# Performance work log

Measured on AMD Instinct MI355X. Metric: run time of the kernel, lower is better.

Reference implementation:

```python
import jax, jax.numpy as jnp
import numpy as np

HEADS = 4
DIM_HEAD = 32
HIDDEN = HEADS * DIM_HEAD  # 128
DIM = 128
RANK = 4
SCALING = 1.0 / RANK       # alpha / rank
SCALE = DIM_HEAD ** -0.5


def conv1x1(x, w, b=None):
    # x: [b,c,H,W], w: [o,c] (1x1 conv kernel squeezed)
    y = jnp.einsum('bcxy,oc->boxy', x, w)
    if b is not None:
        y = y + b[None, :, None, None]
    return y


def setup_inputs() -> dict:
    key = jax.random.key(0)
    ks = jax.random.split(key, 16)
    x = jax.random.normal(ks[0], (16, DIM, 64, 64), dtype=jnp.float32)
    w_qkv = jax.random.normal(ks[1], (3 * HIDDEN, DIM), dtype=jnp.float32) * 0.05
    def lora(kA, kB, kb):
        wA = jax.random.normal(kA, (RANK, DIM), dtype=jnp.float32) / RANK
        bA = jax.random.normal(kB, (RANK,), dtype=jnp.float32) * 0.01
        wB = jax.random.normal(kb, (HIDDEN, RANK), dtype=jnp.float32) * 0.05
        bB = jnp.zeros((HIDDEN,), dtype=jnp.float32)
        return wA, bA, wB, bB
    wA_q, bA_q, wB_q, bB_q = lora(ks[2], ks[3], ks[4])
    wA_k, bA_k, wB_k, bB_k = lora(ks[5], ks[6], ks[7])
    wA_v, bA_v, wB_v, bB_v = lora(ks[8], ks[9], ks[10])
    w_out = jax.random.normal(ks[11], (DIM, HIDDEN), dtype=jnp.float32) * 0.05
    b_out = jnp.zeros((DIM,), dtype=jnp.float32)
    return dict(x=x, w_qkv=w_qkv,
                wA_q=wA_q, bA_q=bA_q, wB_q=wB_q, bB_q=bB_q,
                wA_k=wA_k, bA_k=bA_k, wB_k=wB_k, bB_k=bB_k,
                wA_v=wA_v, bA_v=bA_v, wB_v=wB_v, bB_v=bB_v,
                w_out=w_out, b_out=b_out)


def reference(x, w_qkv, wA_q, bA_q, wB_q, bB_q, wA_k, bA_k, wB_k, bB_k,
              wA_v, bA_v, wB_v, bB_v, w_out, b_out):
    b, c, H, W = x.shape
    n = H * W
    qkv = conv1x1(x, w_qkv)  # [b, 3*HIDDEN, H, W]
    q0, k0, v0 = jnp.split(qkv, 3, axis=1)
    def lora_fwd(wA, bA, wB, bB):
        return conv1x1(conv1x1(x, wA, bA), wB, bB)
    q = q0 + lora_fwd(wA_q, bA_q, wB_q, bB_q) * SCALING
    k = k0 + lora_fwd(wA_k, bA_k, wB_k, bB_k) * SCALING
    v = v0 + lora_fwd(wA_v, bA_v, wB_v, bB_v) * SCALING
    # b (h c) x y -> b h c n
    def split_heads(t):
        return t.reshape(b, HEADS, DIM_HEAD, n)
    q, k, v = split_heads(q), split_heads(k), split_heads(v)
    q = jax.nn.softmax(q, axis=-2) * SCALE   # softmax over channel dim
    k = jax.nn.softmax(k, axis=-1)           # softmax over spatial dim
    v = v / n
    context = jnp.einsum('bhdn,bhen->bhde', k, v)
    out = jnp.einsum('bhde,bhdn->bhen', context, q)  # [b,h,e,n]
    out = out.reshape(b, HIDDEN, H, W)
    return conv1x1(out, w_out, b_out)
```

## Files before the change

### kernel.cpp

```cpp
#include <hip/hip_runtime.h>


typedef float f32x4 __attribute__((ext_vector_type(4)));
typedef short bf16x8 __attribute__((ext_vector_type(8)));

#define SCALING 0.25f
#define SCALE   0.17677669529663687f
#define NCHUNK  64

__device__ __forceinline__ unsigned short f2bf_rn(float x) {
    union { float f; unsigned u; } v; v.f = x;
    unsigned r = v.u + 0x7FFFu + ((v.u >> 16) & 1u);
    return (unsigned short)(r >> 16);
}
__device__ __forceinline__ float bf2f(unsigned short h) {
    union { unsigned u; float f; } v; v.u = ((unsigned)h) << 16;
    return v.f;
}
__device__ __forceinline__ void hilo2(float a, float b, unsigned& hi, unsigned& lo) {
    unsigned short ah = f2bf_rn(a), bh = f2bf_rn(b);
    unsigned short al = f2bf_rn(a - bf2f(ah)), bl = f2bf_rn(b - bf2f(bh));
    hi = (unsigned)ah | ((unsigned)bh << 16);
    lo = (unsigned)al | ((unsigned)bl << 16);
}
__device__ __forceinline__ unsigned pack2(float a, float b) {
    return (unsigned)f2bf_rn(a) | ((unsigned)f2bf_rn(b) << 16);
}

__device__ __forceinline__ float weff(
    const float* __restrict__ w_qkv, const float* __restrict__ wA,
    const float* __restrict__ wB, int m, int o, int c)
{
    float s = w_qkv[(m * 128 + o) * 128 + c];
    #pragma unroll
    for (int r = 0; r < 4; ++r)
        s += SCALING * wB[o * 4 + r] * wA[r * 128 + c];
    return s;
}

__global__ __launch_bounds__(256) void prep_kernel(
    const float* __restrict__ w_qkv,
    const float* __restrict__ wA_q, const float* __restrict__ bA_q,
    const float* __restrict__ wB_q, const float* __restrict__ bB_q,
    const float* __restrict__ wA_k, const float* __restrict__ bA_k,
    const float* __restrict__ wB_k, const float* __restrict__ bB_k,
    const float* __restrict__ wA_v, const float* __restrict__ bA_v,
    const float* __restrict__ wB_v, const float* __restrict__ bB_v,
    unsigned* __restrict__ wq, unsigned* __restrict__ wkv,
    float* __restrict__ beff)
{
    const int t = threadIdx.x;
    if (blockIdx.x == 96) {
        for (int ii = t; ii < 384; ii += 256) {
            int mm = ii >> 7, oo = ii & 127;
            const float* wBm = (mm == 0) ? wB_q : (mm == 1) ? wB_k : wB_v;
            const float* bAm = (mm == 0) ? bA_q : (mm == 1) ? bA_k : bA_v;
            const float* bBm = (mm == 0) ? bB_q : (mm == 1) ? bB_k : bB_v;
            float bb = bBm[oo];
            #pragma unroll
            for (int r = 0; r < 4; ++r) bb += wBm[oo * 4 + r] * bAm[r];
            beff[ii] = SCALING * bb;
        }
        return;
    }
    int tid = blockIdx.x * 256 + t;
    if (tid < 8192) {
        int fp = tid;
        int f = fp * 2;
        int i = f & 7;
        int l = (f >> 3) & 63;
        int rgks = f >> 9;
        int rg = rgks >> 2, ks = rgks & 3;
        int o = rg * 16 + (l & 15);
        int c = ks * 32 + ((l >> 4) & 3) * 8 + i;
        wq[fp] = pack2(weff(w_qkv, wA_q, wB_q, 0, o, c),
                       weff(w_qkv, wA_q, wB_q, 0, o, c + 1));
    } else {
        int fp = tid - 8192;
        int f = fp * 2;
        int i = f & 7;
        int l = (f >> 3) & 63;
        int rtks = f >> 9;
        int rt = rtks >> 2, ks = rtks & 3;
        int row = rt * 16 + (l & 15);
        int c = ks * 32 + ((l >> 4) & 3) * 8 + i;
        int m = 1 + (row >> 7), o = row & 127;
        const float* wA = (m == 1) ? wA_k : wA_v;
        const float* wB = (m == 1) ? wB_k : wB_v;
        wkv[fp] = pack2(weff(w_qkv, wA, wB, m, o, c),
                        weff(w_qkv, wA, wB, m, o, c + 1));
    }
}

__global__ __launch_bounds__(256) void ctx_fused_kernel(
    const float* __restrict__ x, const unsigned* __restrict__ wq,
    const unsigned* __restrict__ wkv, const float* __restrict__ beff,
    float* __restrict__ part, uint4* __restrict__ qs)
{
    __shared__ __align__(16) char smem[36864];
    uint4* xs = (uint4*)smem;
    unsigned short* kv = (unsigned short*)smem;
    const int t = threadIdx.x;
    const int lane = t & 63;
    const int w = __builtin_amdgcn_readfirstlane(t >> 6);
    const int chunk = blockIdx.x, b = blockIdx.y;
    const int lg = lane >> 4, l15 = lane & 15;
    const float* xb = x + (size_t)b * (128 * 4096);
    const int n0 = chunk * 64;
    const uint4* wq4 = (const uint4*)wq;
    const uint4* wkv4 = (const uint4*)wkv;

    #pragma unroll
    for (int p = 0; p < 4; ++p) {
        int g = p * 4 + w;
        float v[8];
        #pragma unroll
        for (int j = 0; j < 8; ++j)
            v[j] = xb[(size_t)(g * 8 + j) * 4096 + n0 + lane];
        xs[g * 64 + lane] = make_uint4(
            pack2(v[0], v[1]), pack2(v[2], v[3]),
            pack2(v[4], v[5]), pack2(v[6], v[7]));
    }
    __syncthreads();

    {
        f32x4 acc[2][4];
        #pragma unroll
        for (int rt = 0; rt < 2; ++rt)
            #pragma unroll
            for (int nt = 0; nt < 4; ++nt)
                acc[rt][nt] = (f32x4){0.f, 0.f, 0.f, 0.f};
        #pragma unroll
        for (int ks = 0; ks < 4; ++ks) {
            bf16x8 bh[4];
            #pragma unroll
            for (int nt = 0; nt < 4; ++nt)
                bh[nt] = __builtin_bit_cast(bf16x8, xs[(ks * 4 + lg) * 64 + nt * 16 + l15]);
            #pragma unroll
            for (int rt = 0; rt < 2; ++rt) {
                bf16x8 ah = __builtin_bit_cast(bf16x8,
                    wq4[((2 * w + rt) * 4 + ks) * 64 + lane]);
                #pragma unroll
                for (int nt = 0; nt < 4; ++nt)
                    acc[rt][nt] = __builtin_amdgcn_mfma_f32_16x16x32_bf16(ah, bh[nt], acc[rt][nt], 0, 0, 0);
            }
        }
        float bq[2][4];
        #pragma unroll
        for (int rt = 0; rt < 2; ++rt)
            #pragma unroll
            for (int r = 0; r < 4; ++r)
                bq[rt][r] = beff[w * 32 + rt * 16 + lg * 4 + r];
        #pragma unroll
        for (int nt = 0; nt < 4; ++nt) {
            float m = -1e30f;
            #pragma unroll
            for (int rt = 0; rt < 2; ++rt)
                #pragma unroll
                for (int r = 0; r < 4; ++r) {
                    float q = acc[rt][nt][r] + bq[rt][r];
                    acc[rt][nt][r] = q;
                    m = fmaxf(m, q);
                }
            m = fmaxf(m, __shfl_xor(m, 16));
            m = fmaxf(m, __shfl_xor(m, 32));
            float s = 0.f;
            #pragma unroll
            for (int rt = 0; rt < 2; ++rt)
                #pragma unroll
                for (int r = 0; r < 4; ++r) {
                    float e = __expf(acc[rt][nt][r] - m);
                    acc[rt][nt][r] = e;
                    s += e;
                }
            s += __shfl_xor(s, 16);
            s += __shfl_xor(s, 32);
            float inv = 1.0f / s;
            #pragma unroll
            for (int rt = 0; rt < 2; ++rt)
                #pragma unroll
                for (int r = 0; r < 4; ++r)
                    acc[rt][nt][r] *= inv;
        }
        uint2* q2g = (uint2*)(qs + ((size_t)b * 64 + chunk) * 1024);
        int half = (lg & 1);
        #pragma unroll
        for (int rt = 0; rt < 2; ++rt) {
            int kb = rt * 2 + (lg >> 1);
            #pragma unroll
            for (int nt = 0; nt < 4; ++nt) {
                int idx = ((w * 4 + kb) * 64 + nt * 16 + l15) * 2 + half;
                q2g[idx] = make_uint2(pack2(acc[rt][nt][0], acc[rt][nt][1]),
                                      pack2(acc[rt][nt][2], acc[rt][nt][3]));
            }
        }
    }

    unsigned pk[4][8];
    #pragma unroll
    for (int rt = 0; rt < 4; ++rt) {
        f32x4 acc[4];
        #pragma unroll
        for (int nt = 0; nt < 4; ++nt) acc[nt] = (f32x4){0.f, 0.f, 0.f, 0.f};
        #pragma unroll
        for (int ks = 0; ks < 4; ++ks) {
            bf16x8 ah = __builtin_bit_cast(bf16x8,
                wkv4[((4 * w + rt) * 4 + ks) * 64 + lane]);
            #pragma unroll
            for (int nt = 0; nt < 4; ++nt) {
                bf16x8 bh = __builtin_bit_cast(bf16x8,
                    xs[(ks * 4 + lg) * 64 + nt * 16 + l15]);
                acc[nt] = __builtin_amdgcn_mfma_f32_16x16x32_bf16(ah, bh, acc[nt], 0, 0, 0);
            }
        }
        #pragma unroll
        for (int nt = 0; nt < 4; ++nt) {
            float v0 = acc[nt][0], v1 = acc[nt][1];
            float v2 = acc[nt][2], v3 = acc[nt][3];
            if (w < 2) {
                v0 = __expf(v0); v1 = __expf(v1);
                v2 = __expf(v2); v3 = __expf(v3);
            }
            pk[rt][nt * 2]     = pack2(v0, v1);
            pk[rt][nt * 2 + 1] = pack2(v2, v3);
        }
    }
    __syncthreads();
    #pragma unroll
    for (int rt = 0; rt < 4; ++rt)
        #pragma unroll
        for (int nt = 0; nt < 4; ++nt)
            #pragma unroll
            for (int rr = 0; rr < 2; ++rr) {
                unsigned u = pk[rt][nt * 2 + rr];
                int row0 = 64 * w + 16 * rt + lg * 4 + rr * 2;
                int px = nt * 16 + l15;
                kv[row0 * 72 + px] = (unsigned short)u;
                kv[(row0 + 1) * 72 + px] = (unsigned short)(u >> 16);
            }
    __syncthreads();

    bf16x8 ones;
    #pragma unroll
    for (int i = 0; i < 8; ++i) ones[i] = (short)0x3F80;
    f32x4 ctx_acc[2][2];
    f32x4 l_acc[2];
    #pragma unroll
    for (int rt = 0; rt < 2; ++rt) {
        l_acc[rt] = (f32x4){0.f, 0.f, 0.f, 0.f};
        #pragma unroll
        for (int et = 0; et < 2; ++et)
            ctx_acc[rt][et] = (f32x4){0.f, 0.f, 0.f, 0.f};
    }
    #pragma unroll
    for (int ks2 = 0; ks2 < 2; ++ks2) {
        int pxb = ks2 * 32 + lg * 8;
        bf16x8 ph[2], vh[2];
        #pragma unroll
        for (int rt = 0; rt < 2; ++rt)
            ph[rt] = __builtin_bit_cast(bf16x8, *(const uint4*)&kv[(32 * w + 16 * rt + l15) * 72 + pxb]);
        #pragma unroll
        for (int et = 0; et < 2; ++et)
            vh[et] = __builtin_bit_cast(bf16x8, *(const uint4*)&kv[(128 + 32 * w + 16 * et + l15) * 72 + pxb]);
        #pragma unroll
        for (int rt = 0; rt < 2; ++rt) {
            #pragma unroll
            for (int et = 0; et < 2; ++et)
                ctx_acc[rt][et] = __builtin_amdgcn_mfma_f32_16x16x32_bf16(ph[rt], vh[et], ctx_acc[rt][et], 0, 0, 0);
            l_acc[rt] = __builtin_amdgcn_mfma_f32_16x16x32_bf16(ph[rt], ones, l_acc[rt], 0, 0, 0);
        }
    }
    float* pout = part + (size_t)((b * 4 + w) * NCHUNK + chunk) * 1056;
    #pragma unroll
    for (int rt = 0; rt < 2; ++rt) {
        #pragma unroll
        for (int et = 0; et < 2; ++et)
            #pragma unroll
            for (int r = 0; r < 4; ++r)
                pout[(16 * rt + lg * 4 + r) * 32 + 16 * et + l15] = ctx_acc[rt][et][r];
        if (l15 == 0)
            #pragma unroll
            for (int r = 0; r < 4; ++r)
                pout[1024 + 16 * rt + lg * 4 + r] = l_acc[rt][r];
    }
}

__global__ __launch_bounds__(256) void combine_a_kernel(
    const float* __restrict__ part, float* __restrict__ part2)
{
    const int t = threadIdx.x;
    const int h = blockIdx.x, b = blockIdx.y, g = blockIdx.z;
    const float* pb = part + (size_t)((b * 4 + h) * NCHUNK + g * 8) * 1056;
    float s[4] = {0.f, 0.f, 0.f, 0.f};
    #pragma unroll 1
    for (int ch = 0; ch < 8; ++ch) {
        #pragma unroll
        for (int i = 0; i < 4; ++i)
            s[i] += pb[(size_t)ch * 1056 + i * 256 + t];
    }
    float* po = part2 + (size_t)(((b * 4 + h) * 8) + g) * 1056;
    #pragma unroll
    for (int i = 0; i < 4; ++i) po[i * 256 + t] = s[i];
    if (t < 32) {
        float l = 0.f;
        #pragma unroll
        for (int ch = 0; ch < 8; ++ch) l += pb[(size_t)ch * 1056 + 1024 + t];
        po[1024 + t] = l;
    }
}

__global__ __launch_bounds__(256) void combine_b_kernel(
    const float* __restrict__ part2, const float* __restrict__ w_out,
    const float* __restrict__ beff,
    unsigned* __restrict__ mhi, unsigned* __restrict__ mlo)
{
    __shared__ float ctx_s[32 * 33];
    __shared__ float w_s[128 * 33];
    __shared__ float linv_s[32];
    __shared__ float bv_s[32];
    const int t = threadIdx.x;
    const int h = blockIdx.x, b = blockIdx.y;
    const float* pb = part2 + (size_t)((b * 4 + h) * 8) * 1056;

    if (t < 32) {
        float l = 0.f;
        #pragma unroll
        for (int p = 0; p < 8; ++p) l += pb[(size_t)p * 1056 + 1024 + t];
        linv_s[t] = 1.0f / (l * 4096.0f);
        bv_s[t] = beff[256 + h * 32 + t];
    }
    #pragma unroll
    for (int i = 0; i < 16; ++i) {
        int idx = i * 256 + t;
        int e = idx & 31, o = idx >> 5;
        w_s[o * 33 + e] = w_out[o * 128 + h * 32 + e];
    }
    float csum[4] = {0.f, 0.f, 0.f, 0.f};
    #pragma unroll
    for (int p = 0; p < 8; ++p) {
        #pragma unroll
        for (int i = 0; i < 4; ++i)
            csum[i] += pb[(size_t)p * 1056 + i * 256 + t];
    }
    __syncthreads();
    #pragma unroll
    for (int i = 0; i < 4; ++i) {
        int idx = i * 256 + t;
        int d = idx >> 5, e = idx & 31;
        ctx_s[d * 33 + e] = csum[i] * linv_s[d] + bv_s[e] * (1.0f / 4096.0f);
    }
    __syncthreads();
    #pragma unroll 1
    for (int it = 0; it < 8; ++it) {
        int p = it * 256 + t;
        int rt = p >> 8;
        int l = (p >> 2) & 63;
        int ip = p & 3;
        int o = rt * 16 + (l & 15);
        int d0 = (l >> 4) * 8 + 2 * ip;
        float v0 = 0.f, v1 = 0.f;
        #pragma unroll
        for (int e = 0; e < 32; ++e) {
            float wv = w_s[o * 33 + e];
            v0 = fmaf(wv, ctx_s[d0 * 33 + e], v0);
            v1 = fmaf(wv, ctx_s[(d0 + 1) * 33 + e], v1);
        }
        v0 *= SCALE; v1 *= SCALE;
        unsigned hi, lo;
        hilo2(v0, v1, hi, lo);
        size_t fp = (size_t)b * 8192 + ((rt * 4 + h) * 64 + l) * 4 + ip;
        mhi[fp] = hi;
        mlo[fp] = lo;
    }
}

__global__ __launch_bounds__(256) void out_kernel(
    const uint4* __restrict__ qs,
    const unsigned* __restrict__ mhi, const unsigned* __restrict__ mlo,
    const float* __restrict__ b_out, float* __restrict__ out)
{
    __shared__ float bias_o[128];
    const int t = threadIdx.x;
    const int tile = blockIdx.x, b = blockIdx.y;
    const int lane = t & 63;
    const int w = __builtin_amdgcn_readfirstlane(t >> 6);
    const int lg = lane >> 4, l15 = lane & 15;
    if (t < 128) bias_o[t] = b_out[t];
    __syncthreads();

    const uint4* q4 = qs + ((size_t)b * 64 + tile) * 1024;
    const uint4* mh4 = (const uint4*)(mhi + (size_t)b * 8192);
    const uint4* ml4 = (const uint4*)(mlo + (size_t)b * 8192);
    f32x4 acc2[2][4];
    #pragma unroll
    for (int rt = 0; rt < 2; ++rt)
        #pragma unroll
        for (int nt = 0; nt < 4; ++nt)
            acc2[rt][nt] = (f32x4){0.f, 0.f, 0.f, 0.f};
    #pragma unroll
    for (int ks = 0; ks < 4; ++ks) {
        bf16x8 bh[4];
        #pragma unroll
        for (int nt = 0; nt < 4; ++nt)
            bh[nt] = __builtin_bit_cast(bf16x8, q4[(ks * 4 + lg) * 64 + nt * 16 + l15]);
        #pragma unroll
        for (int rt = 0; rt < 2; ++rt) {
            int rg = 2 * w + rt;
            bf16x8 ah = __builtin_bit_cast(bf16x8, mh4[(rg * 4 + ks) * 64 + lane]);
            bf16x8 al = __builtin_bit_cast(bf16x8, ml4[(rg * 4 + ks) * 64 + lane]);
            #pragma unroll
            for (int nt = 0; nt < 4; ++nt) {
                acc2[rt][nt] = __builtin_amdgcn_mfma_f32_16x16x32_bf16(ah, bh[nt], acc2[rt][nt], 0, 0, 0);
                acc2[rt][nt] = __builtin_amdgcn_mfma_f32_16x16x32_bf16(al, bh[nt], acc2[rt][nt], 0, 0, 0);
            }
        }
    }
    float* ob = out + (size_t)b * (128 * 4096) + tile * 64;
    #pragma unroll
    for (int rt = 0; rt < 2; ++rt)
        #pragma unroll
        for (int r = 0; r < 4; ++r) {
            int ch = w * 32 + rt * 16 + lg * 4 + r;
            float bo = bias_o[ch];
            #pragma unroll
            for (int nt = 0; nt < 4; ++nt)
                ob[(size_t)ch * 4096 + nt * 16 + l15] = acc2[rt][nt][r] + bo;
        }
}

extern "C" void kernel_launch(void* const* d_in, const int* in_sizes, int n_in,
                              void* d_out, int out_size, void* d_ws, size_t ws_size,
                              hipStream_t stream) {
    const float* x     = (const float*)d_in[0];
    const float* w_qkv = (const float*)d_in[1];
    const float* wA_q  = (const float*)d_in[2];
    const float* bA_q  = (const float*)d_in[3];
    const float* wB_q  = (const float*)d_in[4];
    const float* bB_q  = (const float*)d_in[5];
    const float* wA_k  = (const float*)d_in[6];
    const float* bA_k  = (const float*)d_in[7];
    const float* wB_k  = (const float*)d_in[8];
    const float* bB_k  = (const float*)d_in[9];
    const float* wA_v  = (const float*)d_in[10];
    const float* bA_v  = (const float*)d_in[11];
    const float* wB_v  = (const float*)d_in[12];
    const float* bB_v  = (const float*)d_in[13];
    const float* w_out = (const float*)d_in[14];
    const float* b_out = (const float*)d_in[15];
    float* out = (float*)d_out;

    float* ws = (float*)d_ws;
    float*    beff  = ws;
    float*    part  = ws + 384;
    float*    part2 = ws + 4325760;
    unsigned* wq    = (unsigned*)(ws + 4866432);
    unsigned* wkv   = (unsigned*)(ws + 4874624);
    unsigned* mhi   = (unsigned*)(ws + 4891008);
    unsigned* mlo   = (unsigned*)(ws + 5022080);
    uint4*    qs    = (uint4*)(ws + 5153152);

    prep_kernel<<<97, 256, 0, stream>>>(w_qkv,
        wA_q, bA_q, wB_q, bB_q, wA_k, bA_k, wB_k, bB_k, wA_v, bA_v, wB_v, bB_v,
        wq, wkv, beff);
    ctx_fused_kernel<<<dim3(NCHUNK, 16), 256, 0, stream>>>(x, wq, wkv, beff,
        part, qs);
    combine_a_kernel<<<dim3(4, 16, 8), 256, 0, stream>>>(part, part2);
    combine_b_kernel<<<dim3(4, 16), 256, 0, stream>>>(part2, w_out, beff, mhi, mlo);
    out_kernel<<<dim3(64, 16), 256, 0, stream>>>(qs, mhi, mlo, b_out, out);
}
```

Measured before the change: 54.68 us.

## Drop hi/lo bf16 split for output matrix, split out_kernel tiles, batch x loads

The fused output matrix is now stored as a single bf16 pack instead of a hi/lo pair, which halves the MFMA count and matrix loads in out_kernel. out_kernel now launches twice as many blocks, each covering half of a 64-column chunk, to raise parallelism. The x staging loop in ctx_fused_kernel issues 16 loads before packing, for more memory-level parallelism. The cost is lower precision in the output projection, since the bf16 residual correction is removed.

```diff
diff --git a/kernel.cpp b/kernel.cpp
--- a/kernel.cpp
+++ b/kernel.cpp
@@ -12,16 +12,6 @@
     union { float f; unsigned u; } v; v.f = x;
     unsigned r = v.u + 0x7FFFu + ((v.u >> 16) & 1u);
     return (unsigned short)(r >> 16);
-}
-__device__ __forceinline__ float bf2f(unsigned short h) {
-    union { unsigned u; float f; } v; v.u = ((unsigned)h) << 16;
-    return v.f;
-}
-__device__ __forceinline__ void hilo2(float a, float b, unsigned& hi, unsigned& lo) {
-    unsigned short ah = f2bf_rn(a), bh = f2bf_rn(b);
-    unsigned short al = f2bf_rn(a - bf2f(ah)), bl = f2bf_rn(b - bf2f(bh));
-    hi = (unsigned)ah | ((unsigned)bh << 16);
-    lo = (unsigned)al | ((unsigned)bl << 16);
 }
 __device__ __forceinline__ unsigned pack2(float a, float b) {
     return (unsigned)f2bf_rn(a) | ((unsigned)f2bf_rn(b) << 16);
@@ -111,15 +101,22 @@
     const uint4* wkv4 = (const uint4*)wkv;
 
     #pragma unroll
-    for (int p = 0; p < 4; ++p) {
-        int g = p * 4 + w;
-        float v[8];
-        #pragma unroll
-        for (int j = 0; j < 8; ++j)
-            v[j] = xb[(size_t)(g * 8 + j) * 4096 + n0 + lane];
-        xs[g * 64 + lane] = make_uint4(
-            pack2(v[0], v[1]), pack2(v[2], v[3]),
-            pack2(v[4], v[5]), pack2(v[6], v[7]));
+    for (int pp = 0; pp < 2; ++pp) {
+        float v[16];
+        #pragma unroll
+        for (int g2 = 0; g2 < 2; ++g2) {
+            int g = (pp * 2 + g2) * 4 + w;
+            #pragma unroll
+            for (int j = 0; j < 8; ++j)
+                v[g2 * 8 + j] = xb[(size_t)(g * 8 + j) * 4096 + n0 + lane];
+        }
+        #pragma unroll
+        for (int g2 = 0; g2 < 2; ++g2) {
+            int g = (pp * 2 + g2) * 4 + w;
+            xs[g * 64 + lane] = make_uint4(
+                pack2(v[g2*8+0], v[g2*8+1]), pack2(v[g2*8+2], v[g2*8+3]),
+                pack2(v[g2*8+4], v[g2*8+5]), pack2(v[g2*8+6], v[g2*8+7]));
+        }
     }
     __syncthreads();
 
@@ -311,8 +308,7 @@
 
 __global__ __launch_bounds__(256) void combine_b_kernel(
     const float* __restrict__ part2, const float* __restrict__ w_out,
-    const float* __restrict__ beff,
-    unsigned* __restrict__ mhi, unsigned* __restrict__ mlo)
+    const float* __restrict__ beff, unsigned* __restrict__ mpk)
 {
     __shared__ float ctx_s[32 * 33];
     __shared__ float w_s[128 * 33];
@@ -365,57 +361,51 @@
             v0 = fmaf(wv, ctx_s[d0 * 33 + e], v0);
             v1 = fmaf(wv, ctx_s[(d0 + 1) * 33 + e], v1);
         }
-        v0 *= SCALE; v1 *= SCALE;
-        unsigned hi, lo;
-        hilo2(v0, v1, hi, lo);
         size_t fp = (size_t)b * 8192 + ((rt * 4 + h) * 64 + l) * 4 + ip;
-        mhi[fp] = hi;
-        mlo[fp] = lo;
+        mpk[fp] = pack2(v0 * SCALE, v1 * SCALE);
     }
 }
 
 __global__ __launch_bounds__(256) void out_kernel(
-    const uint4* __restrict__ qs,
-    const unsigned* __restrict__ mhi, const unsigned* __restrict__ mlo,
+    const uint4* __restrict__ qs, const unsigned* __restrict__ mpk,
     const float* __restrict__ b_out, float* __restrict__ out)
 {
     __shared__ float bias_o[128];
     const int t = threadIdx.x;
-    const int tile = blockIdx.x, b = blockIdx.y;
+    const int tile32 = blockIdx.x, b = blockIdx.y;
+    const int chunk = tile32 >> 1;
+    const int nb = (tile32 & 1) * 2;
     const int lane = t & 63;
     const int w = __builtin_amdgcn_readfirstlane(t >> 6);
     const int lg = lane >> 4, l15 = lane & 15;
     if (t < 128) bias_o[t] = b_out[t];
     __syncthreads();
 
-    const uint4* q4 = qs + ((size_t)b * 64 + tile) * 1024;
-    const uint4* mh4 = (const uint4*)(mhi + (size_t)b * 8192);
-    const uint4* ml4 = (const uint4*)(mlo + (size_t)b * 8192);
-    f32x4 acc2[2][4];
+    const uint4* q4 = qs + ((size_t)b * 64 + chunk) * 1024;
+    const uint4* mp4 = (const uint4*)(mpk + (size_t)b * 8192);
+    f32x4 acc2[2][2];
     #pragma unroll
     for (int rt = 0; rt < 2; ++rt)
         #pragma unroll
-        for (int nt = 0; nt < 4; ++nt)
-            acc2[rt][nt] = (f32x4){0.f, 0.f, 0.f, 0.f};
+        for (int n2 = 0; n2 < 2; ++n2)
+            acc2[rt][n2] = (f32x4){0.f, 0.f, 0.f, 0.f};
     #pragma unroll
     for (int ks = 0; ks < 4; ++ks) {
-        bf16x8 bh[4];
-        #pragma unroll
-        for (int nt = 0; nt < 4; ++nt)
-            bh[nt] = __builtin_bit_cast(bf16x8, q4[(ks * 4 + lg) * 64 + nt * 16 + l15]);
+        bf16x8 bh[2];
+        #pragma unroll
+        for (int n2 = 0; n2 < 2; ++n2)
+            bh[n2] = __builtin_bit_cast(bf16x8,
+                q4[(ks * 4 + lg) * 64 + (nb + n2) * 16 + l15]);
         #pragma unroll
         for (int rt = 0; rt < 2; ++rt) {
-            int rg = 2 * w + rt;
-            bf16x8 ah = __builtin_bit_cast(bf16x8, mh4[(rg * 4 + ks) * 64 + lane]);
-            bf16x8 al = __builtin_bit_cast(bf16x8, ml4[(rg * 4 + ks) * 64 + lane]);
-            #pragma unroll
-            for (int nt = 0; nt < 4; ++nt) {
-                acc2[rt][nt] = __builtin_amdgcn_mfma_f32_16x16x32_bf16(ah, bh[nt], acc2[rt][nt], 0, 0, 0);
-                acc2[rt][nt] = __builtin_amdgcn_mfma_f32_16x16x32_bf16(al, bh[nt], acc2[rt][nt], 0, 0, 0);
-            }
-        }
-    }
-    float* ob = out + (size_t)b * (128 * 4096) + tile * 64;
+            bf16x8 ah = __builtin_bit_cast(bf16x8,
+                mp4[((2 * w + rt) * 4 + ks) * 64 + lane]);
+            #pragma unroll
+            for (int n2 = 0; n2 < 2; ++n2)
+                acc2[rt][n2] = __builtin_amdgcn_mfma_f32_16x16x32_bf16(ah, bh[n2], acc2[rt][n2], 0, 0, 0);
+        }
+    }
+    float* ob = out + (size_t)b * (128 * 4096) + chunk * 64;
     #pragma unroll
     for (int rt = 0; rt < 2; ++rt)
         #pragma unroll
@@ -423,8 +413,8 @@
             int ch = w * 32 + rt * 16 + lg * 4 + r;
             float bo = bias_o[ch];
             #pragma unroll
-            for (int nt = 0; nt < 4; ++nt)
-                ob[(size_t)ch * 4096 + nt * 16 + l15] = acc2[rt][nt][r] + bo;
+            for (int n2 = 0; n2 < 2; ++n2)
+                ob[(size_t)ch * 4096 + (nb + n2) * 16 + l15] = acc2[rt][n2][r] + bo;
         }
 }
 
@@ -455,9 +445,8 @@
     float*    part2 = ws + 4325760;
     unsigned* wq    = (unsigned*)(ws + 4866432);
     unsigned* wkv   = (unsigned*)(ws + 4874624);
-    unsigned* mhi   = (unsigned*)(ws + 4891008);
-    unsigned* mlo   = (unsigned*)(ws + 5022080);
-    uint4*    qs    = (uint4*)(ws + 5153152);
+    unsigned* mpk   = (unsigned*)(ws + 4891008);
+    uint4*    qs    = (uint4*)(ws + 5022080);
 
     prep_kernel<<<97, 256, 0, stream>>>(w_qkv,
         wA_q, bA_q, wB_q, bB_q, wA_k, bA_k, wB_k, bB_k, wA_v, bA_v, wB_v, bB_v,
@@ -465,6 +454,6 @@
     ctx_fused_kernel<<<dim3(NCHUNK, 16), 256, 0, stream>>>(x, wq, wkv, beff,
         part, qs);
     combine_a_kernel<<<dim3(4, 16, 8), 256, 0, stream>>>(part, part2);
-    combine_b_kernel<<<dim3(4, 16), 256, 0, stream>>>(part2, w_out, beff, mhi, mlo);
-    out_kernel<<<dim3(64, 16), 256, 0, stream>>>(qs, mhi, mlo, b_out, out);
-}
+    combine_b_kernel<<<dim3(4, 16), 256, 0, stream>>>(part2, w_out, beff, mpk);
+    out_kernel<<<dim3(128, 16), 256, 0, stream>>>(qs, mpk, b_out, out);
+}
```

After: 54.12 us, median of 2. About the same (-1.0%).
